# Performance work log

Measured on AMD Instinct MI355X. Metric: run time of the kernel, lower is better.

Reference implementation:

```python
import math
import jax, jax.numpy as jnp
import numpy as np

DIM = 1024
NUM_HEADS = 16
HEAD_DIM = DIM // NUM_HEADS


def rotate_half(x):
    x1, x2 = jnp.split(x, 2, axis=-1)
    return jnp.concatenate((-x2, x1), axis=-1)


def rope_cos_sin(seq_len, head_dim, dtype):
    # angles: (S, D/2); duplicated to (S, D) so it applies to full head_dim
    pos = jnp.arange(seq_len, dtype=dtype)[:, None]
    inv = jnp.exp(jnp.arange(0, head_dim, 2, dtype=dtype) * (-(math.log(10000.0) / head_dim)))
    angles = pos * inv[None, :]
    angles = jnp.concatenate((angles, angles), axis=-1)  # (S, D)
    return jnp.cos(angles), jnp.sin(angles)


def setup_inputs() -> dict:
    key = jax.random.key(0)
    ks = jax.random.split(key, 5)
    B, S, C = 8, 1024, DIM
    scale = 1.0 / math.sqrt(C)
    return {
        "x": jax.random.normal(ks[0], (B, S, C), dtype=jnp.float32),
        "W_qkv": jax.random.normal(ks[1], (C, 3 * C), dtype=jnp.float32) * scale,
        "b_qkv": jax.random.normal(ks[2], (3 * C,), dtype=jnp.float32) * 0.02,
        "W_proj": jax.random.normal(ks[3], (C, C), dtype=jnp.float32) * scale,
        "b_proj": jax.random.normal(ks[4], (C,), dtype=jnp.float32) * 0.02,
    }


def reference(x, W_qkv, b_qkv, W_proj, b_proj):
    B, S, C = x.shape
    H, D = NUM_HEADS, C // NUM_HEADS
    scale = D ** -0.5

    qkv = x @ W_qkv + b_qkv                       # (B, S, 3C)
    qkv = qkv.reshape(B, S, 3, H, D).transpose(2, 0, 3, 1, 4)  # (3, B, H, S, D)
    q, k, v = qkv[0], qkv[1], qkv[2]

    cos, sin = rope_cos_sin(S, D, x.dtype)        # (S, D) each, broadcast over B,H
    q = q * cos + rotate_half(q) * sin
    k = k * cos + rotate_half(k) * sin

    attn = jnp.einsum("bhqd,bhkd->bhqk", q, k) * scale
    attn = jax.nn.softmax(attn, axis=-1)
    out = jnp.einsum("bhqk,bhkd->bhqd", attn, v)  # (B, H, S, D)
    out = out.transpose(0, 2, 1, 3).reshape(B, S, C)
    return out @ W_proj + b_proj
```

## Files before the change

kernel.cpp:

```cpp
#include <hip/hip_runtime.h>
#include <hip/hip_fp16.h>
#include <math.h>


typedef _Float16 half_t;
typedef _Float16 half8 __attribute__((ext_vector_type(8)));
typedef _Float16 half4v __attribute__((ext_vector_type(4)));
typedef float f32x4 __attribute__((ext_vector_type(4)));

#define MFMA16(a, b, c) __builtin_amdgcn_mfma_f32_16x16x32_f16(a, b, c, 0, 0, 0)

__device__ __forceinline__ void gload_lds16(const half_t* g, half_t* lds) {
  __builtin_amdgcn_global_load_lds(
      (const __attribute__((address_space(1))) void*)g,
      (__attribute__((address_space(3))) void*)lds, 16, 0, 0);
}

__device__ __forceinline__ void prep_transpose(const float* __restrict__ in,
                                               half_t* __restrict__ out,
                                               int rows, int cols, int bx,
                                               int by, half_t (*tile)[33]) {
  int c0 = bx * 32, r0 = by * 32;
  int tx = threadIdx.x & 31, g = threadIdx.x >> 5;
#pragma unroll
  for (int i = 0; i < 4; i++) {
    int r = g * 4 + i;
    tile[r][tx] = (half_t)in[(size_t)(r0 + r) * cols + c0 + tx];
  }
  __syncthreads();
#pragma unroll
  for (int i = 0; i < 4; i++) {
    int cc = g * 4 + i;
    out[(size_t)(c0 + cc) * rows + r0 + tx] = tile[tx][cc];
  }
}

__global__ __launch_bounds__(256) void k_prep(
    const float* __restrict__ x, half_t* __restrict__ x16,
    const float* __restrict__ Wqkv, half_t* __restrict__ WqkvT,
    const float* __restrict__ Wproj, half_t* __restrict__ WprojT,
    float2* __restrict__ rope) {
  __shared__ half_t tile[32][33];
  int bid = blockIdx.x;
  if (bid < 8192) {
    int i = bid * 256 + threadIdx.x;
    float4 v = ((const float4*)x)[i];
    half4v h;
    h.x = (half_t)v.x; h.y = (half_t)v.y; h.z = (half_t)v.z; h.w = (half_t)v.w;
    ((half4v*)x16)[i] = h;
  } else if (bid < 11264) {
    int idx = bid - 8192;
    prep_transpose(Wqkv, WqkvT, 1024, 3072, idx % 96, idx / 96, tile);
  } else if (bid < 12288) {
    int idx = bid - 11264;
    prep_transpose(Wproj, WprojT, 1024, 1024, idx & 31, idx >> 5, tile);
  } else {
    int idx = (bid - 12288) * 256 + threadIdx.x;
    int s = idx >> 5, jj = idx & 31;
    float inv = expf(-0.28782313662425572f * (float)jj);
    float ang = (float)s * inv;
    float sn, cs;
    sincosf(ang, &sn, &cs);
    rope[idx] = make_float2(cs, sn);
  }
}


#define STAGE_HALF(TT, PH)                                                   \
  {                                                                          \
    const int op_ = (PH) & 1, kh_ = (PH) >> 1;                               \
    const half_t* src_ = op_ ? Bt : A;                                       \
    const int r0_ = op_ ? n0 : m0;                                           \
    half_t* reg_ = smem + (((TT) & 1) * 32768) + op_ * 16384 + kh_ * 8192;   \
    _Pragma("unroll") for (int c_ = 0; c_ < 2; ++c_) {                       \
      int gid_ = c_ * 512 + w * 64 + lane;                                   \
      int row_ = gid_ >> 2, gi_ = gid_ & 3;                                  \
      int sg_ = gi_ ^ ((row_ >> 1) & 3);                                     \
      gload_lds16(src_ + (size_t)(r0_ + row_) * 1024 + (TT) * 64 +           \
                      kh_ * 32 + sg_ * 8,                                    \
                  reg_ + (c_ * 512 + w * 64) * 8);                           \
    }                                                                        \
  }

__global__ __launch_bounds__(512, 2) void k_qkv(
    const half_t* __restrict__ A, const half_t* __restrict__ Bt,
    const float* __restrict__ bias, const float2* __restrict__ rope,
    half_t* __restrict__ Qo, half_t* __restrict__ Ko,
    half_t* __restrict__ Vo) {
  __shared__ alignas(16) half_t smem[65536];
  const int t = threadIdx.x;
  const int lane = t & 63, w = t >> 6;
  const int quad = lane >> 4, cl = lane & 15;
  const int wr = w >> 2, wc = w & 3;

  const int bid = blockIdx.x;
  const int wg = (bid & 7) * 48 + (bid >> 3);
  const int m0 = (wg & 31) * 256, n0 = (wg >> 5) * 256;

#pragma unroll
  for (int ph = 0; ph < 4; ++ph) STAGE_HALF(0, ph);
  asm volatile("s_waitcnt vmcnt(4)" ::: "memory");
  __builtin_amdgcn_s_barrier();

  f32x4 acc[8][4] = {};
  half8 bf[4];

  for (int tt = 0; tt < 16; ++tt) {
    half_t* Ab = smem + (tt & 1) * 32768;
    half_t* Bb = Ab + 16384;
#pragma unroll
    for (int ph = 0; ph < 4; ++ph) {
      const int ks = ph >> 1, mh = ph & 1;
      if (mh == 0) {
#pragma unroll
        for (int j = 0; j < 4; ++j) {
          int nr = wc * 64 + j * 16 + cl;
          bf[j] = *(const half8*)(Bb + ks * 8192 + nr * 32 +
                                  ((quad ^ ((nr >> 1) & 3)) * 8));
        }
      }
      half8 af[4];
#pragma unroll
      for (int i = 0; i < 4; ++i) {
        int mr = wr * 128 + mh * 64 + i * 16 + cl;
        af[i] = *(const half8*)(Ab + ks * 8192 + mr * 32 +
                                ((quad ^ ((mr >> 1) & 3)) * 8));
      }
      if (tt < 15) STAGE_HALF(tt + 1, ph);
      __builtin_amdgcn_s_barrier();
      asm volatile("s_waitcnt lgkmcnt(0)" ::: "memory");
      __builtin_amdgcn_sched_barrier(0);
      __builtin_amdgcn_s_setprio(1);
#pragma unroll
      for (int i = 0; i < 4; ++i)
#pragma unroll
        for (int j = 0; j < 4; ++j)
          acc[mh * 4 + i][j] = MFMA16(af[i], bf[j], acc[mh * 4 + i][j]);
      __builtin_amdgcn_s_setprio(0);
      if (ph & 1) {
        if (tt < 15)
          asm volatile("s_waitcnt vmcnt(4)" ::: "memory");
        else
          asm volatile("s_waitcnt vmcnt(0)" ::: "memory");
      }
      __builtin_amdgcn_s_barrier();
    }
  }

  const int which = n0 >> 10;
  const int b = m0 >> 10, sbase = m0 & 1023;
  if (which == 2) {
    half_t* T = smem;
    for (int rm = 0; rm < 2; ++rm) {
      if (rm) __syncthreads();
      if (wr == rm) {
#pragma unroll
        for (int mi = 0; mi < 8; ++mi)
#pragma unroll
          for (int j = 0; j < 4; ++j) {
            int nl = wc * 64 + j * 16 + cl;
            float bs = bias[n0 + nl];
#pragma unroll
            for (int r = 0; r < 4; ++r)
              T[nl * 136 + mi * 16 + quad * 4 + r] =
                  (half_t)(acc[mi][j][r] + bs);
          }
      }
      __syncthreads();
#pragma unroll
      for (int u = 0; u < 8; ++u) {
        int ci = u * 512 + t;
        int nl = ci >> 4, ch = (ci & 15) * 8;
        half8 val = *(const half8*)(T + nl * 136 + ch);
        int n = n0 + nl, hh = (n >> 6) & 15, d = n & 63;
        *(half8*)(Vo + ((size_t)((b * 16 + hh) * 64 + d)) * 1024 + sbase +
                  rm * 128 + ch) = val;
      }
    }
  } else {
    half_t* T = smem;
    const float qsc = (which == 0) ? 0.125f : 1.0f;
    half_t* dst = (which == 0) ? Qo : Ko;
    for (int rm = 0; rm < 2; ++rm) {
      if (rm) __syncthreads();
      if (wr == rm) {
#pragma unroll
        for (int mi = 0; mi < 8; ++mi)
#pragma unroll
          for (int r = 0; r < 4; ++r) {
            int tl = mi * 16 + quad * 4 + r;
            int s = sbase + rm * 128 + tl;
#pragma unroll
            for (int j = 0; j < 4; ++j) {
              int nl = wc * 64 + j * 16 + cl;
              int n = n0 + nl, d = n & 63;
              float v = acc[mi][j][r] + bias[n];
              float pr = acc[mi][j ^ 2][r] + bias[n ^ 32];
              float2 tr = rope[(s << 5) | (d & 31)];
              float rv =
                  (d < 32) ? (v * tr.x - pr * tr.y) : (v * tr.x + pr * tr.y);
              T[tl * 264 + nl] = (half_t)(rv * qsc);
            }
          }
      }
      __syncthreads();
#pragma unroll
      for (int u = 0; u < 8; ++u) {
        int ci = u * 512 + t;
        int mrow = ci >> 5, ch = (ci & 31) * 8;
        half8 val = *(const half8*)(T + mrow * 264 + ch);
        int s = sbase + rm * 128 + mrow;
        int n = n0 + ch, hh = (n >> 6) & 15, d = n & 63;
        *(half8*)(dst + ((size_t)((b * 16 + hh) * 1024 + s)) * 64 + d) = val;
      }
    }
  }
}
#undef STAGE_HALF

template <int MODE>
__global__ __launch_bounds__(256) void k_gemm(
    const half_t* __restrict__ A, const half_t* __restrict__ Bt,
    const float* __restrict__ bias, const float2* __restrict__ rope,
    half_t* __restrict__ Qo, half_t* __restrict__ Ko, half_t* __restrict__ Vo,
    float* __restrict__ Fo) {
  __shared__ alignas(16) half_t smem[17408];
  half_t* As = smem;
  half_t* Bs = smem + 8192;
  const int t = threadIdx.x;
  const int lane = t & 63, w = t >> 6;
  const int quad = lane >> 4, cl = lane & 15;
  const int m0 = blockIdx.y * 128, n0 = blockIdx.x * 128;
  const int wm = (w >> 1) * 64, wn = (w & 1) * 64;

  f32x4 acc[4][4] = {};

  for (int kt = 0; kt < 1024; kt += 64) {
    __syncthreads();
#pragma unroll
    for (int cc = 0; cc < 4; cc++) {
      int lg = (w * 4 + cc) * 64 + lane;
      int row = lg >> 3;
      int gs = (lg & 7) ^ (row & 7);
      gload_lds16(A + (size_t)(m0 + row) * 1024 + kt + gs * 8,
                  As + (w * 4 + cc) * 512);
      gload_lds16(Bt + (size_t)(n0 + row) * 1024 + kt + gs * 8,
                  Bs + (w * 4 + cc) * 512);
    }
    __syncthreads();
#pragma unroll
    for (int ks = 0; ks < 2; ks++) {
      half8 af[4], bf[4];
#pragma unroll
      for (int i = 0; i < 4; i++) {
        int mr = wm + i * 16 + cl;
        af[i] = *(const half8*)(As + mr * 64 + (((ks * 4 + quad) ^ (mr & 7)) * 8));
        int nr = wn + i * 16 + cl;
        bf[i] = *(const half8*)(Bs + nr * 64 + (((ks * 4 + quad) ^ (nr & 7)) * 8));
      }
#pragma unroll
      for (int i = 0; i < 4; i++)
#pragma unroll
        for (int j = 0; j < 4; j++) acc[i][j] = MFMA16(af[i], bf[j], acc[i][j]);
    }
  }

#pragma unroll
  for (int i = 0; i < 4; i++)
#pragma unroll
    for (int r = 0; r < 4; r++) {
      int gm = m0 + wm + i * 16 + quad * 4 + r;
#pragma unroll
      for (int j = 0; j < 4; j++) {
        int n = n0 + wn + j * 16 + cl;
        Fo[(size_t)gm * 1024 + n] = acc[i][j][r] + bias[n];
      }
    }
}

__global__ __launch_bounds__(256) void k_attn(const half_t* __restrict__ Qg_,
                                              const half_t* __restrict__ Kg_,
                                              const half_t* __restrict__ Vg_,
                                              half_t* __restrict__ Og) {
  __shared__ alignas(16) half_t Qs[8192];
  __shared__ alignas(16) half_t Ks[4096];
  __shared__ alignas(16) half_t Vs[4096];
  __shared__ alignas(16) half_t Ps[128 * 72];
  __shared__ float ilbuf[128];
  const int t = threadIdx.x, lane = t & 63, w = t >> 6;
  const int quad = lane >> 4, cl = lane & 15;
  const int bh = blockIdx.x, q0 = blockIdx.y * 128;
  const half_t* Qg = Qg_ + (size_t)bh * 65536;
  const half_t* Kg = Kg_ + (size_t)bh * 65536;
  const half_t* Vg = Vg_ + (size_t)bh * 65536;

#pragma unroll
  for (int cc = 0; cc < 4; cc++) {
    int lg = (w * 4 + cc) * 64 + lane;
    int row = lg >> 3;
    int gs = (lg & 7) ^ (row & 7);
    gload_lds16(Qg + (size_t)(q0 + row) * 64 + gs * 8, Qs + (w * 4 + cc) * 512);
  }
  __syncthreads();

  half8 qf[2][2];
#pragma unroll
  for (int ks = 0; ks < 2; ks++)
#pragma unroll
    for (int j = 0; j < 2; j++) {
      int qr = w * 32 + j * 16 + cl;
      qf[ks][j] = *(const half8*)(Qs + qr * 64 + (((ks * 4 + quad) ^ (qr & 7)) * 8));
    }

  f32x4 oacc[2][4] = {};
  float lsum[2] = {0.f, 0.f};

  for (int kt = 0; kt < 1024; kt += 64) {
    __syncthreads();
#pragma unroll
    for (int cc = 0; cc < 2; cc++) {
      int lg = (w * 2 + cc) * 64 + lane;
      int row = lg >> 3;
      int gs = (lg & 7) ^ (row & 7);
      gload_lds16(Kg + (size_t)(kt + row) * 64 + gs * 8, Ks + (w * 2 + cc) * 512);
      gload_lds16(Vg + (size_t)row * 1024 + kt + gs * 8, Vs + (w * 2 + cc) * 512);
    }
    __syncthreads();

    f32x4 sacc[4][2] = {};
#pragma unroll
    for (int ks = 0; ks < 2; ks++) {
      half8 kf[4];
#pragma unroll
      for (int i = 0; i < 4; i++) {
        int kr = i * 16 + cl;
        kf[i] = *(const half8*)(Ks + kr * 64 + (((ks * 4 + quad) ^ (kr & 7)) * 8));
      }
#pragma unroll
      for (int i = 0; i < 4; i++)
#pragma unroll
        for (int j = 0; j < 2; j++)
          sacc[i][j] = MFMA16(kf[i], qf[ks][j], sacc[i][j]);
    }

#pragma unroll
    for (int i = 0; i < 4; i++)
#pragma unroll
      for (int j = 0; j < 2; j++) {
        float p0 = __expf(sacc[i][j][0] - 8.f);
        float p1 = __expf(sacc[i][j][1] - 8.f);
        float p2 = __expf(sacc[i][j][2] - 8.f);
        float p3 = __expf(sacc[i][j][3] - 8.f);
        lsum[j] += (p0 + p1) + (p2 + p3);
        half4v pk;
        pk.x = (half_t)p0; pk.y = (half_t)p1; pk.z = (half_t)p2; pk.w = (half_t)p3;
        *(half4v*)(Ps + (w * 32 + j * 16 + cl) * 72 + i * 16 + quad * 4) = pk;
      }

#pragma unroll
    for (int ks = 0; ks < 2; ks++) {
      half8 pf[2], vf[4];
#pragma unroll
      for (int i = 0; i < 2; i++)
        pf[i] = *(const half8*)(Ps + (w * 32 + i * 16 + cl) * 72 + ks * 32 + quad * 8);
#pragma unroll
      for (int j = 0; j < 4; j++) {
        int dr = j * 16 + cl;
        vf[j] = *(const half8*)(Vs + dr * 64 + (((ks * 4 + quad) ^ (dr & 7)) * 8));
      }
#pragma unroll
      for (int i = 0; i < 2; i++)
#pragma unroll
        for (int j = 0; j < 4; j++) oacc[i][j] = MFMA16(pf[i], vf[j], oacc[i][j]);
    }
  }

#pragma unroll
  for (int j = 0; j < 2; j++) {
    float l = lsum[j];
    l += __shfl_xor(l, 16);
    l += __shfl_xor(l, 32);
    if (quad == 0) ilbuf[w * 32 + j * 16 + cl] = 1.f / l;
  }

  const int b = bh >> 4, hh = bh & 15;
#pragma unroll
  for (int i = 0; i < 2; i++)
#pragma unroll
    for (int r = 0; r < 4; r++) {
      float sc = ilbuf[w * 32 + i * 16 + quad * 4 + r];
      int srow = q0 + w * 32 + i * 16 + quad * 4 + r;
#pragma unroll
      for (int j = 0; j < 4; j++) {
        int d = j * 16 + cl;
        Og[((size_t)(b * 1024 + srow)) * 1024 + hh * 64 + d] =
            (half_t)(oacc[i][j][r] * sc);
      }
    }
}

extern "C" void kernel_launch(void* const* d_in, const int* in_sizes, int n_in,
                              void* d_out, int out_size, void* d_ws,
                              size_t ws_size, hipStream_t stream) {
  (void)in_sizes; (void)n_in; (void)out_size; (void)ws_size;
  const float* x = (const float*)d_in[0];
  const float* Wqkv = (const float*)d_in[1];
  const float* bqkv = (const float*)d_in[2];
  const float* Wproj = (const float*)d_in[3];
  const float* bproj = (const float*)d_in[4];
  float* out = (float*)d_out;

  half_t* ws = (half_t*)d_ws;
  half_t* x16 = ws;
  half_t* WqkvT = ws + 8388608;
  half_t* WprojT = ws + 11534336;
  half_t* Q16 = ws + 12582912;
  half_t* K16 = ws + 20971520;
  half_t* V16 = ws + 29360128;
  float2* rope = (float2*)(ws + 37748736);
  half_t* O16 = x16;

  k_prep<<<12416, 256, 0, stream>>>(x, x16, Wqkv, WqkvT, Wproj, WprojT, rope);
  k_qkv<<<384, 512, 0, stream>>>(x16, WqkvT, bqkv, rope, Q16, K16, V16);
  k_attn<<<dim3(128, 8), 256, 0, stream>>>(Q16, K16, V16, O16);
  k_gemm<1><<<dim3(8, 64), 256, 0, stream>>>(O16, WprojT, bproj, nullptr,
                                             nullptr, nullptr, nullptr, out);
}
```

Before: 301.1 us.

## Restructure QKV GEMM pipeline and double-buffer projection GEMM

The QKV GEMM replaces its fine-grained four-phase staging, which used manual vmcnt waits and per-phase barriers, with a simpler scheme. It now prefetches the whole next 64-wide K tile into the other LDS buffer, runs the MFMAs, and syncs once per tile, using a new 8-way XOR swizzle layout. The projection GEMM becomes a dedicated kernel with double-buffered LDS (larger shared memory), prefetching the next tile while computing, with raised MFMA priority. The aim is fewer barriers and overlap of global-to-LDS loads with compute in the projection. In exchange, the QKV kernel gives up its finer-grained overlap, and the projection kernel's bigger LDS footprint may lower occupancy.

```diff
diff --git a/kernel.cpp b/kernel.cpp
--- a/kernel.cpp
+++ b/kernel.cpp
@@ -65,22 +65,18 @@
   }
 }
 
-
-#define STAGE_HALF(TT, PH)                                                   \
-  {                                                                          \
-    const int op_ = (PH) & 1, kh_ = (PH) >> 1;                               \
-    const half_t* src_ = op_ ? Bt : A;                                       \
-    const int r0_ = op_ ? n0 : m0;                                           \
-    half_t* reg_ = smem + (((TT) & 1) * 32768) + op_ * 16384 + kh_ * 8192;   \
-    _Pragma("unroll") for (int c_ = 0; c_ < 2; ++c_) {                       \
-      int gid_ = c_ * 512 + w * 64 + lane;                                   \
-      int row_ = gid_ >> 2, gi_ = gid_ & 3;                                  \
-      int sg_ = gi_ ^ ((row_ >> 1) & 3);                                     \
-      gload_lds16(src_ + (size_t)(r0_ + row_) * 1024 + (TT) * 64 +           \
-                      kh_ * 32 + sg_ * 8,                                    \
-                  reg_ + (c_ * 512 + w * 64) * 8);                           \
-    }                                                                        \
-  }
+__device__ __forceinline__ void qkv_stage(const half_t* __restrict__ A,
+                                          const half_t* __restrict__ Bt,
+                                          int m0, int n0, int rowp, int gsp,
+                                          int w, int kt, half_t* db) {
+#pragma unroll
+  for (int c = 0; c < 4; ++c) {
+    gload_lds16(A + (size_t)(m0 + c * 64 + rowp) * 1024 + kt + gsp * 8,
+                db + c * 4096 + w * 512);
+    gload_lds16(Bt + (size_t)(n0 + c * 64 + rowp) * 1024 + kt + gsp * 8,
+                db + 16384 + c * 4096 + w * 512);
+  }
+}
 
 __global__ __launch_bounds__(512, 2) void k_qkv(
     const half_t* __restrict__ A, const half_t* __restrict__ Bt,
@@ -92,59 +88,53 @@
   const int lane = t & 63, w = t >> 6;
   const int quad = lane >> 4, cl = lane & 15;
   const int wr = w >> 2, wc = w & 3;
+  const int rowp = t >> 3;
+  const int gsp = (t & 7) ^ ((t >> 3) & 7);
+  const int xsw = cl & 7;
 
   const int bid = blockIdx.x;
   const int wg = (bid & 7) * 48 + (bid >> 3);
   const int m0 = (wg & 31) * 256, n0 = (wg >> 5) * 256;
 
-#pragma unroll
-  for (int ph = 0; ph < 4; ++ph) STAGE_HALF(0, ph);
-  asm volatile("s_waitcnt vmcnt(4)" ::: "memory");
-  __builtin_amdgcn_s_barrier();
+  qkv_stage(A, Bt, m0, n0, rowp, gsp, w, 0, smem);
+  __syncthreads();
 
   f32x4 acc[8][4] = {};
-  half8 bf[4];
-
+
+#pragma unroll 2
   for (int tt = 0; tt < 16; ++tt) {
     half_t* Ab = smem + (tt & 1) * 32768;
     half_t* Bb = Ab + 16384;
-#pragma unroll
-    for (int ph = 0; ph < 4; ++ph) {
-      const int ks = ph >> 1, mh = ph & 1;
-      if (mh == 0) {
-#pragma unroll
-        for (int j = 0; j < 4; ++j) {
-          int nr = wc * 64 + j * 16 + cl;
-          bf[j] = *(const half8*)(Bb + ks * 8192 + nr * 32 +
-                                  ((quad ^ ((nr >> 1) & 3)) * 8));
+    if (tt < 15)
+      qkv_stage(A, Bt, m0, n0, rowp, gsp, w, (tt + 1) * 64,
+                smem + ((tt + 1) & 1) * 32768);
+    __builtin_amdgcn_sched_barrier(0);
+#pragma unroll
+    for (int ks = 0; ks < 2; ++ks) {
+      half8 bf[4];
+#pragma unroll
+      for (int j = 0; j < 4; ++j) {
+        int nr = wc * 64 + j * 16 + cl;
+        bf[j] = *(const half8*)(Bb + nr * 64 + (((ks * 4 + quad) ^ xsw) * 8));
+      }
+#pragma unroll
+      for (int mh = 0; mh < 2; ++mh) {
+        half8 af[4];
+#pragma unroll
+        for (int i = 0; i < 4; ++i) {
+          int mr = wr * 128 + mh * 64 + i * 16 + cl;
+          af[i] = *(const half8*)(Ab + mr * 64 + (((ks * 4 + quad) ^ xsw) * 8));
         }
-      }
-      half8 af[4];
-#pragma unroll
-      for (int i = 0; i < 4; ++i) {
-        int mr = wr * 128 + mh * 64 + i * 16 + cl;
-        af[i] = *(const half8*)(Ab + ks * 8192 + mr * 32 +
-                                ((quad ^ ((mr >> 1) & 3)) * 8));
-      }
-      if (tt < 15) STAGE_HALF(tt + 1, ph);
-      __builtin_amdgcn_s_barrier();
-      asm volatile("s_waitcnt lgkmcnt(0)" ::: "memory");
-      __builtin_amdgcn_sched_barrier(0);
-      __builtin_amdgcn_s_setprio(1);
-#pragma unroll
-      for (int i = 0; i < 4; ++i)
-#pragma unroll
-        for (int j = 0; j < 4; ++j)
-          acc[mh * 4 + i][j] = MFMA16(af[i], bf[j], acc[mh * 4 + i][j]);
-      __builtin_amdgcn_s_setprio(0);
-      if (ph & 1) {
-        if (tt < 15)
-          asm volatile("s_waitcnt vmcnt(4)" ::: "memory");
-        else
-          asm volatile("s_waitcnt vmcnt(0)" ::: "memory");
-      }
-      __builtin_amdgcn_s_barrier();
-    }
+        __builtin_amdgcn_s_setprio(1);
+#pragma unroll
+        for (int i = 0; i < 4; ++i)
+#pragma unroll
+          for (int j = 0; j < 4; ++j)
+            acc[mh * 4 + i][j] = MFMA16(af[i], bf[j], acc[mh * 4 + i][j]);
+        __builtin_amdgcn_s_setprio(0);
+      }
+    }
+    __syncthreads();
   }
 
   const int which = n0 >> 10;
@@ -216,17 +206,28 @@
     }
   }
 }
-#undef STAGE_HALF
-
-template <int MODE>
-__global__ __launch_bounds__(256) void k_gemm(
-    const half_t* __restrict__ A, const half_t* __restrict__ Bt,
-    const float* __restrict__ bias, const float2* __restrict__ rope,
-    half_t* __restrict__ Qo, half_t* __restrict__ Ko, half_t* __restrict__ Vo,
-    float* __restrict__ Fo) {
-  __shared__ alignas(16) half_t smem[17408];
-  half_t* As = smem;
-  half_t* Bs = smem + 8192;
+
+__device__ __forceinline__ void proj_stage(const half_t* __restrict__ A,
+                                           const half_t* __restrict__ Bt,
+                                           int m0, int n0, int w, int lane,
+                                           int kt, half_t* db) {
+#pragma unroll
+  for (int cc = 0; cc < 4; cc++) {
+    int lg = (w * 4 + cc) * 64 + lane;
+    int row = lg >> 3;
+    int gs = (lg & 7) ^ (row & 7);
+    gload_lds16(A + (size_t)(m0 + row) * 1024 + kt + gs * 8,
+                db + (w * 4 + cc) * 512);
+    gload_lds16(Bt + (size_t)(n0 + row) * 1024 + kt + gs * 8,
+                db + 8192 + (w * 4 + cc) * 512);
+  }
+}
+
+__global__ __launch_bounds__(256) void k_proj(const half_t* __restrict__ A,
+                                              const half_t* __restrict__ Bt,
+                                              const float* __restrict__ bias,
+                                              float* __restrict__ Fo) {
+  __shared__ alignas(16) half_t smem[32768];
   const int t = threadIdx.x;
   const int lane = t & 63, w = t >> 6;
   const int quad = lane >> 4, cl = lane & 15;
@@ -235,19 +236,17 @@
 
   f32x4 acc[4][4] = {};
 
-  for (int kt = 0; kt < 1024; kt += 64) {
-    __syncthreads();
-#pragma unroll
-    for (int cc = 0; cc < 4; cc++) {
-      int lg = (w * 4 + cc) * 64 + lane;
-      int row = lg >> 3;
-      int gs = (lg & 7) ^ (row & 7);
-      gload_lds16(A + (size_t)(m0 + row) * 1024 + kt + gs * 8,
-                  As + (w * 4 + cc) * 512);
-      gload_lds16(Bt + (size_t)(n0 + row) * 1024 + kt + gs * 8,
-                  Bs + (w * 4 + cc) * 512);
-    }
-    __syncthreads();
+  proj_stage(A, Bt, m0, n0, w, lane, 0, smem);
+  __syncthreads();
+
+#pragma unroll 2
+  for (int tt = 0; tt < 16; ++tt) {
+    half_t* As = smem + (tt & 1) * 16384;
+    half_t* Bs = As + 8192;
+    if (tt < 15)
+      proj_stage(A, Bt, m0, n0, w, lane, (tt + 1) * 64,
+                 smem + ((tt + 1) & 1) * 16384);
+    __builtin_amdgcn_sched_barrier(0);
 #pragma unroll
     for (int ks = 0; ks < 2; ks++) {
       half8 af[4], bf[4];
@@ -258,11 +257,14 @@
         int nr = wn + i * 16 + cl;
         bf[i] = *(const half8*)(Bs + nr * 64 + (((ks * 4 + quad) ^ (nr & 7)) * 8));
       }
+      __builtin_amdgcn_s_setprio(1);
 #pragma unroll
       for (int i = 0; i < 4; i++)
 #pragma unroll
         for (int j = 0; j < 4; j++) acc[i][j] = MFMA16(af[i], bf[j], acc[i][j]);
-    }
+      __builtin_amdgcn_s_setprio(0);
+    }
+    __syncthreads();
   }
 
 #pragma unroll
@@ -423,6 +425,5 @@
   k_prep<<<12416, 256, 0, stream>>>(x, x16, Wqkv, WqkvT, Wproj, WprojT, rope);
   k_qkv<<<384, 512, 0, stream>>>(x16, WqkvT, bqkv, rope, Q16, K16, V16);
   k_attn<<<dim3(128, 8), 256, 0, stream>>>(Q16, K16, V16, O16);
-  k_gemm<1><<<dim3(8, 64), 256, 0, stream>>>(O16, WprojT, bproj, nullptr,
-                                             nullptr, nullptr, nullptr, out);
-}
+  k_proj<<<dim3(8, 64), 256, 0, stream>>>(O16, WprojT, bproj, out);
+}
```

New measurement: 294.7 us. -2.1%, faster.
